# Kernel tuning notes

Measured on AMD Instinct MI355X. Metric: run time of the kernel, lower is better.

## Reference

```python
import jax, jax.numpy as jnp
import numpy as np
import math

NUM_HEADS = 8
DIM = 512
DH = DIM // NUM_HEADS  # 64


def _rotary(x):
    # x: (b, l, h, s, d) ; interleaved-pair rotary (lucidrains RotaryEmbedding default)
    d = x.shape[-1]
    s = x.shape[-2]
    inv_freq = 1.0 / (10000.0 ** (jnp.arange(0, d, 2, dtype=jnp.float32) / d))  # (d/2,)
    t = jnp.arange(s, dtype=jnp.float32)
    freqs = t[:, None] * inv_freq[None, :]                # (s, d/2)
    freqs = jnp.repeat(freqs, 2, axis=-1)                 # (s, d) interleaved duplication
    cos = jnp.cos(freqs).astype(x.dtype)
    sin = jnp.sin(freqs).astype(x.dtype)
    x1 = x[..., 0::2]
    x2 = x[..., 1::2]
    rot = jnp.stack([-x2, x1], axis=-1).reshape(x.shape)  # rotate_half on interleaved pairs
    return x * cos + rot * sin


def setup_inputs() -> dict:
    key = jax.random.key(0)
    ks = jax.random.split(key, 9)
    b, l, s = 2, 2, 2048
    std = 1.0 / math.sqrt(DIM)
    inp = {
        "x": jax.random.normal(ks[0], (b, l, s, DIM), dtype=jnp.float32),
        "Wq": jax.random.normal(ks[1], (DIM, DIM), dtype=jnp.float32) * std,
        "bq": jnp.zeros((DIM,), dtype=jnp.float32),
        "Wk": jax.random.normal(ks[2], (DIM, DIM), dtype=jnp.float32) * std,
        "bk": jnp.zeros((DIM,), dtype=jnp.float32),
        "Wv": jax.random.normal(ks[3], (DIM, DIM), dtype=jnp.float32) * std,
        "bv": jnp.zeros((DIM,), dtype=jnp.float32),
        "Wo": jax.random.normal(ks[4], (DIM, DIM), dtype=jnp.float32) * std,
        "bo": jnp.zeros((DIM,), dtype=jnp.float32),
    }
    return inp


def reference(x, Wq, bq, Wk, bk, Wv, bv, Wo, bo):
    b, l, s, _ = x.shape
    h, dh = NUM_HEADS, DH

    def proj(W, bias):
        y = jnp.einsum('blsd,ed->blse', x, W) + bias      # nn.Linear: x @ W.T + b
        return y.reshape(b, l, s, h, dh).transpose(0, 1, 3, 2, 4)  # b l h s d

    q_proj = proj(Wq, bq)
    k_proj = proj(Wk, bk)
    v_proj = proj(Wv, bv)

    # Faithful to the source's swapped tuple unpack: k_mat <- V projection, v_mat <- K projection
    q_mat = _rotary(q_proj)
    k_mat = _rotary(v_proj)
    v_mat = k_proj

    scale = 1.0 / math.sqrt(dh * h)  # sqrt(dim), as in source
    scores = jnp.einsum('blhqd,blhkd->blhqk', q_mat, k_mat) * scale

    causal = jnp.tril(jnp.ones((s, s), dtype=bool))
    scores = jnp.where(causal[None, None, None], scores, -jnp.inf)

    weights = jax.nn.softmax(scores, axis=-1)
    inter = jnp.einsum('blhqk,blhkd->blhqd', weights, v_mat)
    inter = inter.transpose(0, 1, 3, 2, 4).reshape(b, l, s, h * dh)  # b l s (h d)
    out = jnp.einsum('blse,de->blsd', inter, Wo) + bo
    return out
```

## Files before the change

### kernel.cpp

```cpp
#include <hip/hip_runtime.h>
#include <math.h>

#define BB 2
#define LL 2
#define SS 2048
#define DD 512
#define HH 8
#define DHH 64

typedef __attribute__((ext_vector_type(8))) short bf16x8;
typedef __attribute__((ext_vector_type(4))) float f32x4;

#define MFMA16(a, b, c) __builtin_amdgcn_mfma_f32_16x16x32_bf16((a), (b), (c), 0, 0, 0)

#if __has_builtin(__builtin_amdgcn_exp2f)
#define EXP2F(x) __builtin_amdgcn_exp2f(x)
#else
#define EXP2F(x) exp2f(x)
#endif

__device__ __forceinline__ unsigned short f2bf(float f) {
    union { float f; unsigned u; } x; x.f = f;
    unsigned u = x.u;
    return (unsigned short)((u + 0x7fffu + ((u >> 16) & 1u)) >> 16);
}

__device__ __forceinline__ void gload16(const unsigned short* g, unsigned short* l) {
    __builtin_amdgcn_global_load_lds(
        (const __attribute__((address_space(1))) unsigned int*)g,
        (__attribute__((address_space(3))) unsigned int*)l, 16, 0, 0);
}

__global__ void rope_table_kernel(float* __restrict__ cos_t, float* __restrict__ sin_t) {
    int idx = blockIdx.x * 256 + threadIdx.x;
    if (idx >= SS * 32) return;
    int s = idx >> 5;
    int f = idx & 31;
    double inv = pow(10000.0, -(double)(2 * f) / (double)DHH);
    double ang = (double)s * inv;
    cos_t[idx] = (float)cos(ang);
    sin_t[idx] = (float)sin(ang);
}

__global__ __launch_bounds__(256) void convert_kernel(
    const float* __restrict__ x,  const float* __restrict__ wq,
    const float* __restrict__ wk, const float* __restrict__ wv,
    const float* __restrict__ wo, unsigned short* __restrict__ dst)
{
    int i = blockIdx.x * 256 + threadIdx.x;
    const float* src;
    int local;
    if (i < 1048576)      { src = x;  local = i; }
    else if (i < 1114112) { src = wq; local = i - 1048576; }
    else if (i < 1179648) { src = wk; local = i - 1114112; }
    else if (i < 1245184) { src = wv; local = i - 1179648; }
    else                  { src = wo; local = i - 1245184; }
    float4 v = ((const float4*)src)[local];
    ushort4 o;
    o.x = f2bf(v.x); o.y = f2bf(v.y); o.z = f2bf(v.z); o.w = f2bf(v.w);
    *(ushort4*)&dst[(size_t)i * 4] = o;
}

__global__ __launch_bounds__(256) void qkv_mfma_kernel(
    const unsigned short* __restrict__ xb,
    const unsigned short* __restrict__ wqb,
    const unsigned short* __restrict__ wkb,
    const unsigned short* __restrict__ wvb,
    const float* __restrict__ bq, const float* __restrict__ bk,
    const float* __restrict__ bv,
    const float* __restrict__ cos_t, const float* __restrict__ sin_t,
    unsigned short* __restrict__ qm, unsigned short* __restrict__ km,
    unsigned short* __restrict__ vt)
{
    __shared__ __align__(16) unsigned short As[4096];
    __shared__ __align__(16) unsigned short Bs[4096];

    const int tid  = threadIdx.x;
    const int w    = tid >> 6;
    const int lane = tid & 63;
    const int c    = lane & 15;
    const int quad = lane >> 4;
    const int mw   = (w & 1) * 64;
    const int nw   = (w >> 1) * 64;

    const int bx    = blockIdx.x;
    const int mat   = bx >> 2;
    const int nloc0 = (bx & 3) * 128;
    const int row0  = blockIdx.y * 128;

    const unsigned short* wsel = (mat == 0) ? wqb : (mat == 1) ? wkb : wvb;
    const float* bsel          = (mat == 0) ? bq  : (mat == 1) ? bk  : bv;

    const unsigned short* aSrc = (mat == 1) ? (wsel + (size_t)nloc0 * DD)
                                            : (xb   + (size_t)row0  * DD);
    const unsigned short* bSrc = (mat == 1) ? (xb   + (size_t)row0  * DD)
                                            : (wsel + (size_t)nloc0 * DD);

    f32x4 acc[4][4];
    #pragma unroll
    for (int i = 0; i < 4; ++i)
        #pragma unroll
        for (int j = 0; j < 4; ++j)
            #pragma unroll
            for (int r = 0; r < 4; ++r) acc[i][j][r] = 0.f;

    for (int k0 = 0; k0 < DD; k0 += 32) {
        __syncthreads();
        #pragma unroll
        for (int it = 0; it < 2; ++it) {
            int L   = it * 2048 + w * 512 + lane * 8;
            int row = L >> 5;
            int k   = L & 31;
            gload16(aSrc + (size_t)row * DD + k0 + k, &As[L]);
            gload16(bSrc + (size_t)row * DD + k0 + k, &Bs[L]);
        }
        __syncthreads();
        bf16x8 af[4], bfr[4];
        #pragma unroll
        for (int mt = 0; mt < 4; ++mt)
            af[mt] = *(const bf16x8*)&As[(mw + mt * 16 + c) * 32 + quad * 8];
        #pragma unroll
        for (int nt = 0; nt < 4; ++nt)
            bfr[nt] = *(const bf16x8*)&Bs[(nw + nt * 16 + c) * 32 + quad * 8];
        #pragma unroll
        for (int mt = 0; mt < 4; ++mt)
            #pragma unroll
            for (int nt = 0; nt < 4; ++nt)
                acc[mt][nt] = MFMA16(af[mt], bfr[nt], acc[mt][nt]);
    }

    if (mat == 1) {
        #pragma unroll
        for (int mt = 0; mt < 4; ++mt) {
            #pragma unroll
            for (int nt = 0; nt < 4; ++nt) {
                int xr = row0 + nw + nt * 16 + c;
                int bl = xr >> 11, s = xr & 2047;
                #pragma unroll
                for (int r = 0; r < 4; ++r) {
                    int col = nloc0 + mw + mt * 16 + quad * 4 + r;
                    int h = col >> 6, dh = col & 63;
                    float v = acc[mt][nt][r] + bsel[col];
                    vt[((size_t)(bl * HH + h) * DHH + dh) * SS + s] = f2bf(v);
                }
            }
        }
    } else {
        unsigned short* dst = (mat == 0) ? qm : km;
        const float qscale = (mat == 0) ? 0.06375871448932861f : 1.0f;
        #pragma unroll
        for (int mt = 0; mt < 4; ++mt) {
            #pragma unroll
            for (int r = 0; r < 4; ++r) {
                int xr = row0 + mw + mt * 16 + quad * 4 + r;
                int bl = xr >> 11, s = xr & 2047;
                #pragma unroll
                for (int nt = 0; nt < 4; ++nt) {
                    int col = nloc0 + nw + nt * 16 + c;
                    int h = col >> 6, dh = col & 63;
                    float v = acc[mt][nt][r] + bsel[col];
                    float pv = __shfl_xor(v, 1);
                    int f = dh >> 1;
                    float cs = cos_t[s * 32 + f], sn = sin_t[s * 32 + f];
                    float o = (dh & 1) ? fmaf(v, cs, pv * sn)
                                       : fmaf(v, cs, -(pv * sn));
                    dst[((size_t)(bl * HH + h) * SS + s) * DHH + dh] = f2bf(o * qscale);
                }
            }
        }
    }
}

#define S_P 72

__global__ __launch_bounds__(256, 2) void attn_mfma_kernel(
    const unsigned short* __restrict__ qm,
    const unsigned short* __restrict__ km,
    const unsigned short* __restrict__ vt,
    unsigned short* __restrict__ inter)
{
    __shared__ __align__(16) unsigned short Ks[2][4096];
    __shared__ __align__(16) unsigned short Vs[2][4096];
    __shared__ __align__(16) unsigned short Ps[128 * S_P];

    const int tid  = threadIdx.x;
    const int w    = tid >> 6;
    const int lane = tid & 63;
    const int c    = lane & 15;
    const int quad = lane >> 4;

    const int h  = blockIdx.x;
    const int qt = 15 - blockIdx.y;
    const int bl = blockIdx.z;
    const int qw = qt * 128 + w * 32;

    const size_t seq_base = (size_t)(bl * HH + h) * SS * DHH;
    const size_t vt_base  = (size_t)(bl * HH + h) * DHH * SS;

    bf16x8 qf[2][2];
    #pragma unroll
    for (int nt = 0; nt < 2; ++nt)
        #pragma unroll
        for (int kk = 0; kk < 2; ++kk)
            qf[nt][kk] = *(const bf16x8*)(qm + seq_base +
                (size_t)(qw + nt * 16 + c) * DHH + kk * 32 + quad * 8);

    f32x4 oacc[4][2];
    f32x4 lacc[2];
    #pragma unroll
    for (int i = 0; i < 4; ++i)
        #pragma unroll
        for (int j = 0; j < 2; ++j)
            #pragma unroll
            for (int r = 0; r < 4; ++r) oacc[i][j][r] = 0.f;
    #pragma unroll
    for (int j = 0; j < 2; ++j)
        #pragma unroll
        for (int r = 0; r < 4; ++r) lacc[j][r] = 0.f;

    bf16x8 ones;
    #pragma unroll
    for (int i = 0; i < 8; ++i) ones[i] = (short)0x3F80;

    const int ntiles = 2 * qt + 2;

    auto stage = [&](int kt, int b) {
        const unsigned short* kg = km + seq_base + (size_t)(kt * 64) * DHH;
        const unsigned short* vg = vt + vt_base + kt * 64;
        #pragma unroll
        for (int it = 0; it < 2; ++it) {
            int L   = it * 256 + tid;
            int row = L >> 3;
            int gch = (L & 7) ^ (row & 7);
            gload16(kg + row * DHH + gch * 8, &Ks[b][L * 8]);
            gload16(vg + (size_t)row * SS + gch * 8, &Vs[b][L * 8]);
        }
    };

    stage(0, 0);
    __syncthreads();

    for (int kt = 0; kt < ntiles; ++kt) {
        const int b = kt & 1;
        const int ktn = (kt + 1 < ntiles) ? kt + 1 : kt;
        stage(ktn, b ^ 1);

        if (64 * kt <= qw + 31) {
            f32x4 sacc[4][2];
            #pragma unroll
            for (int mt = 0; mt < 4; ++mt)
                #pragma unroll
                for (int nt = 0; nt < 2; ++nt)
                    #pragma unroll
                    for (int r = 0; r < 4; ++r) sacc[mt][nt][r] = 0.f;
            #pragma unroll
            for (int kk = 0; kk < 2; ++kk) {
                bf16x8 kf[4];
                #pragma unroll
                for (int mt = 0; mt < 4; ++mt) {
                    int rr = mt * 16 + c;
                    kf[mt] = *(const bf16x8*)&Ks[b][rr * 64 +
                        (((kk * 4 + quad) ^ (rr & 7)) * 8)];
                }
                #pragma unroll
                for (int mt = 0; mt < 4; ++mt)
                    #pragma unroll
                    for (int nt = 0; nt < 2; ++nt)
                        sacc[mt][nt] = MFMA16(kf[mt], qf[nt][kk], sacc[mt][nt]);
            }

            const bool need_mask = (64 * kt + 63 > qw);
            #pragma unroll
            for (int mt = 0; mt < 4; ++mt) {
                #pragma unroll
                for (int nt = 0; nt < 2; ++nt) {
                    int q = qw + nt * 16 + c;
                    unsigned u[4];
                    #pragma unroll
                    for (int r = 0; r < 4; ++r) {
                        float p = EXP2F(sacc[mt][nt][r]);
                        if (need_mask) {
                            int key = kt * 64 + mt * 16 + quad * 4 + r;
                            if (key > q) p = 0.f;
                        }
                        union { float f; unsigned u; } cv; cv.f = p;
                        u[r] = cv.u + 0x8000u;
                    }
                    uint2 d;
                    d.x = __builtin_amdgcn_perm(u[1], u[0], 0x07060302u);
                    d.y = __builtin_amdgcn_perm(u[3], u[2], 0x07060302u);
                    *(uint2*)&Ps[(w * 32 + nt * 16 + c) * S_P + mt * 16 + quad * 4] = d;
                }
            }

            #pragma unroll
            for (int kk = 0; kk < 2; ++kk) {
                bf16x8 bp[2];
                #pragma unroll
                for (int nt = 0; nt < 2; ++nt) {
                    bp[nt] = *(const bf16x8*)&Ps[(w * 32 + nt * 16 + c) * S_P +
                                                 kk * 32 + quad * 8];
                    lacc[nt] = MFMA16(ones, bp[nt], lacc[nt]);
                }
                #pragma unroll
                for (int mt4 = 0; mt4 < 4; ++mt4) {
                    int rv = mt4 * 16 + c;
                    bf16x8 av = *(const bf16x8*)&Vs[b][rv * 64 +
                        (((kk * 4 + quad) ^ (rv & 7)) * 8)];
                    oacc[mt4][0] = MFMA16(av, bp[0], oacc[mt4][0]);
                    oacc[mt4][1] = MFMA16(av, bp[1], oacc[mt4][1]);
                }
            }
        }
        __syncthreads();
    }

    float invl0 = 1.f / lacc[0][0];
    float invl1 = 1.f / lacc[1][0];
    #pragma unroll
    for (int mt4 = 0; mt4 < 4; ++mt4) {
        int dh0 = mt4 * 16 + quad * 4;
        #pragma unroll
        for (int nt = 0; nt < 2; ++nt) {
            int query = qw + nt * 16 + c;
            float il = nt ? invl1 : invl0;
            ushort4 o;
            o.x = f2bf(oacc[mt4][nt][0] * il);
            o.y = f2bf(oacc[mt4][nt][1] * il);
            o.z = f2bf(oacc[mt4][nt][2] * il);
            o.w = f2bf(oacc[mt4][nt][3] * il);
            *(ushort4*)&inter[((size_t)bl * SS + query) * DD + h * DHH + dh0] = o;
        }
    }
}

__global__ __launch_bounds__(256) void outproj_mfma_kernel(
    const unsigned short* __restrict__ ib,
    const unsigned short* __restrict__ wob,
    const float* __restrict__ bo, float* __restrict__ out)
{
    __shared__ __align__(16) unsigned short As[4096];
    __shared__ __align__(16) unsigned short Bs[4096];

    const int tid  = threadIdx.x;
    const int w    = tid >> 6;
    const int lane = tid & 63;
    const int c    = lane & 15;
    const int quad = lane >> 4;
    const int mw   = (w & 1) * 64;
    const int nw   = (w >> 1) * 64;

    const int n0   = blockIdx.x * 128;
    const int row0 = blockIdx.y * 128;

    const unsigned short* aSrc = ib  + (size_t)row0 * DD;
    const unsigned short* bSrc = wob + (size_t)n0   * DD;

    f32x4 acc[4][4];
    #pragma unroll
    for (int i = 0; i < 4; ++i)
        #pragma unroll
        for (int j = 0; j < 4; ++j)
            #pragma unroll
            for (int r = 0; r < 4; ++r) acc[i][j][r] = 0.f;

    for (int k0 = 0; k0 < DD; k0 += 32) {
        __syncthreads();
        #pragma unroll
        for (int it = 0; it < 2; ++it) {
            int L   = it * 2048 + w * 512 + lane * 8;
            int row = L >> 5;
            int k   = L & 31;
            gload16(aSrc + (size_t)row * DD + k0 + k, &As[L]);
            gload16(bSrc + (size_t)row * DD + k0 + k, &Bs[L]);
        }
        __syncthreads();
        bf16x8 af[4], bfr[4];
        #pragma unroll
        for (int mt = 0; mt < 4; ++mt)
            af[mt] = *(const bf16x8*)&As[(mw + mt * 16 + c) * 32 + quad * 8];
        #pragma unroll
        for (int nt = 0; nt < 4; ++nt)
            bfr[nt] = *(const bf16x8*)&Bs[(nw + nt * 16 + c) * 32 + quad * 8];
        #pragma unroll
        for (int mt = 0; mt < 4; ++mt)
            #pragma unroll
            for (int nt = 0; nt < 4; ++nt)
                acc[mt][nt] = MFMA16(af[mt], bfr[nt], acc[mt][nt]);
    }

    #pragma unroll
    for (int mt = 0; mt < 4; ++mt) {
        #pragma unroll
        for (int r = 0; r < 4; ++r) {
            int xr = row0 + mw + mt * 16 + quad * 4 + r;
            #pragma unroll
            for (int nt = 0; nt < 4; ++nt) {
                int col = n0 + nw + nt * 16 + c;
                out[(size_t)xr * DD + col] = acc[mt][nt][r] + bo[col];
            }
        }
    }
}

extern "C" void kernel_launch(void* const* d_in, const int* in_sizes, int n_in,
                              void* d_out, int out_size, void* d_ws, size_t ws_size,
                              hipStream_t stream)
{
    const float* x  = (const float*)d_in[0];
    const float* Wq = (const float*)d_in[1];
    const float* bq = (const float*)d_in[2];
    const float* Wk = (const float*)d_in[3];
    const float* bk = (const float*)d_in[4];
    const float* Wv = (const float*)d_in[5];
    const float* bv = (const float*)d_in[6];
    const float* Wo = (const float*)d_in[7];
    const float* bo = (const float*)d_in[8];
    float* out = (float*)d_out;
    char* ws = (char*)d_ws;

    unsigned short* inter = (unsigned short*)(ws);
    float* cos_t = (float*)(ws + 8388608);
    float* sin_t = (float*)(ws + 8650752);
    unsigned short* xb  = (unsigned short*)(ws + 8912896);
    unsigned short* wqb = (unsigned short*)(ws + 17301504);
    unsigned short* wkb = (unsigned short*)(ws + 17825792);
    unsigned short* wvb = (unsigned short*)(ws + 18350080);
    unsigned short* wob = (unsigned short*)(ws + 18874368);
    unsigned short* qm  = (unsigned short*)(ws + 19398656);
    unsigned short* km  = (unsigned short*)(ws + 27787264);
    unsigned short* vt  = (unsigned short*)(ws + 36175872);

    rope_table_kernel<<<dim3(256), dim3(256), 0, stream>>>(cos_t, sin_t);
    convert_kernel<<<dim3(5120), dim3(256), 0, stream>>>(x, Wq, Wk, Wv, Wo, xb);
    qkv_mfma_kernel<<<dim3(12, 64), dim3(256), 0, stream>>>(
        xb, wqb, wkb, wvb, bq, bk, bv, cos_t, sin_t, qm, km, vt);
    attn_mfma_kernel<<<dim3(HH, 16, BB * LL), dim3(256), 0, stream>>>(qm, km, vt, inter);
    outproj_mfma_kernel<<<dim3(4, 64), dim3(256), 0, stream>>>(inter, wob, bo, out);
}
```

Before: 192.4 us.

## Double-buffer GEMM loads, shrink attention tiles, merge prep kernels

Merges the rope-table and bf16 conversion kernels into one launch. Adds double-buffered LDS staging with one barrier per k-step to the QKV and output-projection GEMMs. Halves the output-projection N tile to launch more blocks. Cuts attention blocks to 128 threads covering 64 query rows, which doubles the grid and removes the per-wave causal skip. The aim is to hide global-load latency behind MFMA work and to fill more CUs on short causal rows, at the cost of more LDS per block and fewer queries sharing each K/V tile.

```diff
diff --git a/kernel.cpp b/kernel.cpp
--- a/kernel.cpp
+++ b/kernel.cpp
@@ -31,34 +31,34 @@
         (__attribute__((address_space(3))) unsigned int*)l, 16, 0, 0);
 }
 
-__global__ void rope_table_kernel(float* __restrict__ cos_t, float* __restrict__ sin_t) {
-    int idx = blockIdx.x * 256 + threadIdx.x;
-    if (idx >= SS * 32) return;
-    int s = idx >> 5;
-    int f = idx & 31;
-    double inv = pow(10000.0, -(double)(2 * f) / (double)DHH);
-    double ang = (double)s * inv;
-    cos_t[idx] = (float)cos(ang);
-    sin_t[idx] = (float)sin(ang);
-}
-
-__global__ __launch_bounds__(256) void convert_kernel(
+__global__ __launch_bounds__(256) void prep_kernel(
     const float* __restrict__ x,  const float* __restrict__ wq,
     const float* __restrict__ wk, const float* __restrict__ wv,
-    const float* __restrict__ wo, unsigned short* __restrict__ dst)
+    const float* __restrict__ wo, unsigned short* __restrict__ dst,
+    float* __restrict__ cos_t, float* __restrict__ sin_t)
 {
     int i = blockIdx.x * 256 + threadIdx.x;
-    const float* src;
-    int local;
-    if (i < 1048576)      { src = x;  local = i; }
-    else if (i < 1114112) { src = wq; local = i - 1048576; }
-    else if (i < 1179648) { src = wk; local = i - 1114112; }
-    else if (i < 1245184) { src = wv; local = i - 1179648; }
-    else                  { src = wo; local = i - 1245184; }
-    float4 v = ((const float4*)src)[local];
-    ushort4 o;
-    o.x = f2bf(v.x); o.y = f2bf(v.y); o.z = f2bf(v.z); o.w = f2bf(v.w);
-    *(ushort4*)&dst[(size_t)i * 4] = o;
+    if (i < 1310720) {
+        const float* src;
+        int local;
+        if (i < 1048576)      { src = x;  local = i; }
+        else if (i < 1114112) { src = wq; local = i - 1048576; }
+        else if (i < 1179648) { src = wk; local = i - 1114112; }
+        else if (i < 1245184) { src = wv; local = i - 1179648; }
+        else                  { src = wo; local = i - 1245184; }
+        float4 v = ((const float4*)src)[local];
+        ushort4 o;
+        o.x = f2bf(v.x); o.y = f2bf(v.y); o.z = f2bf(v.z); o.w = f2bf(v.w);
+        *(ushort4*)&dst[(size_t)i * 4] = o;
+    } else {
+        int idx = i - 1310720;
+        int s = idx >> 5;
+        int f = idx & 31;
+        double inv = pow(10000.0, -(double)(2 * f) / (double)DHH);
+        double ang = (double)s * inv;
+        cos_t[idx] = (float)cos(ang);
+        sin_t[idx] = (float)sin(ang);
+    }
 }
 
 __global__ __launch_bounds__(256) void qkv_mfma_kernel(
@@ -72,8 +72,8 @@
     unsigned short* __restrict__ qm, unsigned short* __restrict__ km,
     unsigned short* __restrict__ vt)
 {
-    __shared__ __align__(16) unsigned short As[4096];
-    __shared__ __align__(16) unsigned short Bs[4096];
+    __shared__ __align__(16) unsigned short As[2][4096];
+    __shared__ __align__(16) unsigned short Bs[2][4096];
 
     const int tid  = threadIdx.x;
     const int w    = tid >> 6;
@@ -96,6 +96,17 @@
     const unsigned short* bSrc = (mat == 1) ? (xb   + (size_t)row0  * DD)
                                             : (wsel + (size_t)nloc0 * DD);
 
+    auto stage = [&](int k0, int bb) {
+        #pragma unroll
+        for (int it = 0; it < 2; ++it) {
+            int L   = it * 256 + tid;
+            int row = L >> 2;
+            int k8  = (L & 3) * 8;
+            gload16(aSrc + (size_t)row * DD + k0 + k8, &As[bb][L * 8]);
+            gload16(bSrc + (size_t)row * DD + k0 + k8, &Bs[bb][L * 8]);
+        }
+    };
+
     f32x4 acc[4][4];
     #pragma unroll
     for (int i = 0; i < 4; ++i)
@@ -104,29 +115,27 @@
             #pragma unroll
             for (int r = 0; r < 4; ++r) acc[i][j][r] = 0.f;
 
+    stage(0, 0);
+    __syncthreads();
+
     for (int k0 = 0; k0 < DD; k0 += 32) {
-        __syncthreads();
-        #pragma unroll
-        for (int it = 0; it < 2; ++it) {
-            int L   = it * 2048 + w * 512 + lane * 8;
-            int row = L >> 5;
-            int k   = L & 31;
-            gload16(aSrc + (size_t)row * DD + k0 + k, &As[L]);
-            gload16(bSrc + (size_t)row * DD + k0 + k, &Bs[L]);
-        }
-        __syncthreads();
+        const int bb = (k0 >> 5) & 1;
+        if (k0 + 32 < DD) stage(k0 + 32, bb ^ 1);
+
         bf16x8 af[4], bfr[4];
         #pragma unroll
         for (int mt = 0; mt < 4; ++mt)
-            af[mt] = *(const bf16x8*)&As[(mw + mt * 16 + c) * 32 + quad * 8];
+            af[mt] = *(const bf16x8*)&As[bb][(mw + mt * 16 + c) * 32 + quad * 8];
         #pragma unroll
         for (int nt = 0; nt < 4; ++nt)
-            bfr[nt] = *(const bf16x8*)&Bs[(nw + nt * 16 + c) * 32 + quad * 8];
+            bfr[nt] = *(const bf16x8*)&Bs[bb][(nw + nt * 16 + c) * 32 + quad * 8];
         #pragma unroll
         for (int mt = 0; mt < 4; ++mt)
             #pragma unroll
             for (int nt = 0; nt < 4; ++nt)
                 acc[mt][nt] = MFMA16(af[mt], bfr[nt], acc[mt][nt]);
+
+        __syncthreads();
     }
 
     if (mat == 1) {
@@ -173,7 +182,7 @@
 
 #define S_P 72
 
-__global__ __launch_bounds__(256, 2) void attn_mfma_kernel(
+__global__ __launch_bounds__(128) void attn_mfma_kernel(
     const unsigned short* __restrict__ qm,
     const unsigned short* __restrict__ km,
     const unsigned short* __restrict__ vt,
@@ -181,7 +190,7 @@
 {
     __shared__ __align__(16) unsigned short Ks[2][4096];
     __shared__ __align__(16) unsigned short Vs[2][4096];
-    __shared__ __align__(16) unsigned short Ps[128 * S_P];
+    __shared__ __align__(16) unsigned short Ps[64 * S_P];
 
     const int tid  = threadIdx.x;
     const int w    = tid >> 6;
@@ -190,9 +199,9 @@
     const int quad = lane >> 4;
 
     const int h  = blockIdx.x;
-    const int qt = 15 - blockIdx.y;
+    const int qt = 31 - blockIdx.y;
     const int bl = blockIdx.z;
-    const int qw = qt * 128 + w * 32;
+    const int qw = qt * 64 + w * 32;
 
     const size_t seq_base = (size_t)(bl * HH + h) * SS * DHH;
     const size_t vt_base  = (size_t)(bl * HH + h) * DHH * SS;
@@ -222,96 +231,93 @@
     #pragma unroll
     for (int i = 0; i < 8; ++i) ones[i] = (short)0x3F80;
 
-    const int ntiles = 2 * qt + 2;
-
-    auto stage = [&](int kt, int b) {
-        const unsigned short* kg = km + seq_base + (size_t)(kt * 64) * DHH;
-        const unsigned short* vg = vt + vt_base + kt * 64;
-        #pragma unroll
-        for (int it = 0; it < 2; ++it) {
-            int L   = it * 256 + tid;
+    auto stage = [&](int kt, int bb) {
+        const unsigned short* kg = km + seq_base + (size_t)(kt << 6) * DHH;
+        const unsigned short* vg = vt + vt_base + (kt << 6);
+        #pragma unroll
+        for (int it = 0; it < 4; ++it) {
+            int L   = it * 128 + tid;
             int row = L >> 3;
             int gch = (L & 7) ^ (row & 7);
-            gload16(kg + row * DHH + gch * 8, &Ks[b][L * 8]);
-            gload16(vg + (size_t)row * SS + gch * 8, &Vs[b][L * 8]);
+            gload16(kg + row * DHH + gch * 8, &Ks[bb][L * 8]);
+            gload16(vg + (size_t)row * SS + gch * 8, &Vs[bb][L * 8]);
         }
     };
 
+    const int ntiles = qt + 1;
     stage(0, 0);
     __syncthreads();
 
     for (int kt = 0; kt < ntiles; ++kt) {
-        const int b = kt & 1;
-        const int ktn = (kt + 1 < ntiles) ? kt + 1 : kt;
-        stage(ktn, b ^ 1);
-
-        if (64 * kt <= qw + 31) {
-            f32x4 sacc[4][2];
+        const int bb = kt & 1;
+        if (kt + 1 < ntiles) stage(kt + 1, bb ^ 1);
+
+        f32x4 sacc[4][2];
+        #pragma unroll
+        for (int mt = 0; mt < 4; ++mt)
+            #pragma unroll
+            for (int nt = 0; nt < 2; ++nt)
+                #pragma unroll
+                for (int r = 0; r < 4; ++r) sacc[mt][nt][r] = 0.f;
+        #pragma unroll
+        for (int kk = 0; kk < 2; ++kk) {
+            bf16x8 kf[4];
+            #pragma unroll
+            for (int mt = 0; mt < 4; ++mt) {
+                int rr = mt * 16 + c;
+                kf[mt] = *(const bf16x8*)&Ks[bb][rr * 64 +
+                    (((kk * 4 + quad) ^ (rr & 7)) * 8)];
+            }
             #pragma unroll
             for (int mt = 0; mt < 4; ++mt)
                 #pragma unroll
                 for (int nt = 0; nt < 2; ++nt)
-                    #pragma unroll
-                    for (int r = 0; r < 4; ++r) sacc[mt][nt][r] = 0.f;
-            #pragma unroll
-            for (int kk = 0; kk < 2; ++kk) {
-                bf16x8 kf[4];
+                    sacc[mt][nt] = MFMA16(kf[mt], qf[nt][kk], sacc[mt][nt]);
+        }
+
+        const bool need_mask = (64 * kt + 63 > qw);
+        #pragma unroll
+        for (int mt = 0; mt < 4; ++mt) {
+            #pragma unroll
+            for (int nt = 0; nt < 2; ++nt) {
+                int q = qw + nt * 16 + c;
+                unsigned u[4];
                 #pragma unroll
-                for (int mt = 0; mt < 4; ++mt) {
-                    int rr = mt * 16 + c;
-                    kf[mt] = *(const bf16x8*)&Ks[b][rr * 64 +
-                        (((kk * 4 + quad) ^ (rr & 7)) * 8)];
+                for (int r = 0; r < 4; ++r) {
+                    float p = EXP2F(sacc[mt][nt][r]);
+                    if (need_mask) {
+                        int key = kt * 64 + mt * 16 + quad * 4 + r;
+                        if (key > q) p = 0.f;
+                    }
+                    union { float f; unsigned u; } cv; cv.f = p;
+                    u[r] = cv.u + 0x8000u;
                 }
-                #pragma unroll
-                for (int mt = 0; mt < 4; ++mt)
-                    #pragma unroll
-                    for (int nt = 0; nt < 2; ++nt)
-                        sacc[mt][nt] = MFMA16(kf[mt], qf[nt][kk], sacc[mt][nt]);
-            }
-
-            const bool need_mask = (64 * kt + 63 > qw);
-            #pragma unroll
-            for (int mt = 0; mt < 4; ++mt) {
-                #pragma unroll
-                for (int nt = 0; nt < 2; ++nt) {
-                    int q = qw + nt * 16 + c;
-                    unsigned u[4];
-                    #pragma unroll
-                    for (int r = 0; r < 4; ++r) {
-                        float p = EXP2F(sacc[mt][nt][r]);
-                        if (need_mask) {
-                            int key = kt * 64 + mt * 16 + quad * 4 + r;
-                            if (key > q) p = 0.f;
-                        }
-                        union { float f; unsigned u; } cv; cv.f = p;
-                        u[r] = cv.u + 0x8000u;
-                    }
-                    uint2 d;
-                    d.x = __builtin_amdgcn_perm(u[1], u[0], 0x07060302u);
-                    d.y = __builtin_amdgcn_perm(u[3], u[2], 0x07060302u);
-                    *(uint2*)&Ps[(w * 32 + nt * 16 + c) * S_P + mt * 16 + quad * 4] = d;
-                }
-            }
-
-            #pragma unroll
-            for (int kk = 0; kk < 2; ++kk) {
-                bf16x8 bp[2];
-                #pragma unroll
-                for (int nt = 0; nt < 2; ++nt) {
-                    bp[nt] = *(const bf16x8*)&Ps[(w * 32 + nt * 16 + c) * S_P +
-                                                 kk * 32 + quad * 8];
-                    lacc[nt] = MFMA16(ones, bp[nt], lacc[nt]);
-                }
-                #pragma unroll
-                for (int mt4 = 0; mt4 < 4; ++mt4) {
-                    int rv = mt4 * 16 + c;
-                    bf16x8 av = *(const bf16x8*)&Vs[b][rv * 64 +
-                        (((kk * 4 + quad) ^ (rv & 7)) * 8)];
-                    oacc[mt4][0] = MFMA16(av, bp[0], oacc[mt4][0]);
-                    oacc[mt4][1] = MFMA16(av, bp[1], oacc[mt4][1]);
-                }
-            }
-        }
+                uint2 d;
+                d.x = __builtin_amdgcn_perm(u[1], u[0], 0x07060302u);
+                d.y = __builtin_amdgcn_perm(u[3], u[2], 0x07060302u);
+                *(uint2*)&Ps[(w * 32 + nt * 16 + c) * S_P + mt * 16 + quad * 4] = d;
+            }
+        }
+
+        #pragma unroll
+        for (int kk = 0; kk < 2; ++kk) {
+            bf16x8 bp[2];
+            #pragma unroll
+            for (int nt = 0; nt < 2; ++nt) {
+                bp[nt] = *(const bf16x8*)&Ps[(w * 32 + nt * 16 + c) * S_P +
+                                             kk * 32 + quad * 8];
+                lacc[nt] = MFMA16(ones, bp[nt], lacc[nt]);
+            }
+            #pragma unroll
+            for (int mt4 = 0; mt4 < 4; ++mt4) {
+                int rv = mt4 * 16 + c;
+                bf16x8 av = *(const bf16x8*)&Vs[bb][rv * 64 +
+                    (((kk * 4 + quad) ^ (rv & 7)) * 8)];
+                oacc[mt4][0] = MFMA16(av, bp[0], oacc[mt4][0]);
+                oacc[mt4][1] = MFMA16(av, bp[1], oacc[mt4][1]);
+            }
+        }
+
         __syncthreads();
     }
 
@@ -339,8 +345,8 @@
     const unsigned short* __restrict__ wob,
     const float* __restrict__ bo, float* __restrict__ out)
 {
-    __shared__ __align__(16) unsigned short As[4096];
-    __shared__ __align__(16) unsigned short Bs[4096];
+    __shared__ __align__(16) unsigned short As[2][4096];
+    __shared__ __align__(16) unsigned short Bs[2][2048];
 
     const int tid  = threadIdx.x;
     const int w    = tid >> 6;
@@ -348,45 +354,55 @@
     const int c    = lane & 15;
     const int quad = lane >> 4;
     const int mw   = (w & 1) * 64;
-    const int nw   = (w >> 1) * 64;
-
-    const int n0   = blockIdx.x * 128;
+    const int nw   = (w >> 1) * 32;
+
+    const int n0   = blockIdx.x * 64;
     const int row0 = blockIdx.y * 128;
 
     const unsigned short* aSrc = ib  + (size_t)row0 * DD;
     const unsigned short* bSrc = wob + (size_t)n0   * DD;
 
-    f32x4 acc[4][4];
+    auto stage = [&](int k0, int bb) {
+        #pragma unroll
+        for (int it = 0; it < 2; ++it) {
+            int L = it * 256 + tid;
+            gload16(aSrc + (size_t)(L >> 2) * DD + k0 + (L & 3) * 8,
+                    &As[bb][L * 8]);
+        }
+        int L = tid;
+        gload16(bSrc + (size_t)(L >> 2) * DD + k0 + (L & 3) * 8,
+                &Bs[bb][L * 8]);
+    };
+
+    f32x4 acc[4][2];
     #pragma unroll
     for (int i = 0; i < 4; ++i)
         #pragma unroll
-        for (int j = 0; j < 4; ++j)
+        for (int j = 0; j < 2; ++j)
             #pragma unroll
             for (int r = 0; r < 4; ++r) acc[i][j][r] = 0.f;
 
+    stage(0, 0);
+    __syncthreads();
+
     for (int k0 = 0; k0 < DD; k0 += 32) {
+        const int bb = (k0 >> 5) & 1;
+        if (k0 + 32 < DD) stage(k0 + 32, bb ^ 1);
+
+        bf16x8 af[4], bfr[2];
+        #pragma unroll
+        for (int mt = 0; mt < 4; ++mt)
+            af[mt] = *(const bf16x8*)&As[bb][(mw + mt * 16 + c) * 32 + quad * 8];
+        #pragma unroll
+        for (int nt = 0; nt < 2; ++nt)
+            bfr[nt] = *(const bf16x8*)&Bs[bb][(nw + nt * 16 + c) * 32 + quad * 8];
+        #pragma unroll
+        for (int mt = 0; mt < 4; ++mt)
+            #pragma unroll
+            for (int nt = 0; nt < 2; ++nt)
+                acc[mt][nt] = MFMA16(af[mt], bfr[nt], acc[mt][nt]);
+
         __syncthreads();
-        #pragma unroll
-        for (int it = 0; it < 2; ++it) {
-            int L   = it * 2048 + w * 512 + lane * 8;
-            int row = L >> 5;
-            int k   = L & 31;
-            gload16(aSrc + (size_t)row * DD + k0 + k, &As[L]);
-            gload16(bSrc + (size_t)row * DD + k0 + k, &Bs[L]);
-        }
-        __syncthreads();
-        bf16x8 af[4], bfr[4];
-        #pragma unroll
-        for (int mt = 0; mt < 4; ++mt)
-            af[mt] = *(const bf16x8*)&As[(mw + mt * 16 + c) * 32 + quad * 8];
-        #pragma unroll
-        for (int nt = 0; nt < 4; ++nt)
-            bfr[nt] = *(const bf16x8*)&Bs[(nw + nt * 16 + c) * 32 + quad * 8];
-        #pragma unroll
-        for (int mt = 0; mt < 4; ++mt)
-            #pragma unroll
-            for (int nt = 0; nt < 4; ++nt)
-                acc[mt][nt] = MFMA16(af[mt], bfr[nt], acc[mt][nt]);
     }
 
     #pragma unroll
@@ -395,7 +411,7 @@
         for (int r = 0; r < 4; ++r) {
             int xr = row0 + mw + mt * 16 + quad * 4 + r;
             #pragma unroll
-            for (int nt = 0; nt < 4; ++nt) {
+            for (int nt = 0; nt < 2; ++nt) {
                 int col = n0 + nw + nt * 16 + c;
                 out[(size_t)xr * DD + col] = acc[mt][nt][r] + bo[col];
             }
@@ -431,10 +447,10 @@
     unsigned short* km  = (unsigned short*)(ws + 27787264);
     unsigned short* vt  = (unsigned short*)(ws + 36175872);
 
-    rope_table_kernel<<<dim3(256), dim3(256), 0, stream>>>(cos_t, sin_t);
-    convert_kernel<<<dim3(5120), dim3(256), 0, stream>>>(x, Wq, Wk, Wv, Wo, xb);
+    prep_kernel<<<dim3(5376), dim3(256), 0, stream>>>(
+        x, Wq, Wk, Wv, Wo, xb, cos_t, sin_t);
     qkv_mfma_kernel<<<dim3(12, 64), dim3(256), 0, stream>>>(
         xb, wqb, wkb, wvb, bq, bk, bv, cos_t, sin_t, qm, km, vt);
-    attn_mfma_kernel<<<dim3(HH, 16, BB * LL), dim3(256), 0, stream>>>(qm, km, vt, inter);
-    outproj_mfma_kernel<<<dim3(4, 64), dim3(256), 0, stream>>>(inter, wob, bo, out);
-}
+    attn_mfma_kernel<<<dim3(HH, 32, BB * LL), dim3(128), 0, stream>>>(qm, km, vt, inter);
+    outproj_mfma_kernel<<<dim3(8, 64), dim3(256), 0, stream>>>(inter, wob, bo, out);
+}
```

Result: no change. 195.7 us (+1.7%).
